# Performance work log

Hardware: AMD Instinct MI355X
Metric: run time of the kernel (lower is better)

## Reference

```python
import jax, jax.numpy as jnp
import numpy as np

B, C, L = 8, 512, 2048   # batch, input_dim (channels), sequence length
H = 8                    # multihead_cnt
K = 3                    # kernel_dim
DH = C // H              # per-head dim = 64
SCALE = 1.0 / float(np.sqrt(C))  # module divides by sqrt(input_dim), not sqrt(head_dim)


def _conv1d(x, w, b):
    # x: [B, C, L], w: [C_out, C_in, K], padding=1 keeps L
    y = jax.lax.conv_general_dilated(x, w, window_strides=(1,), padding=[(1, 1)],
                                     dimension_numbers=('NCH', 'OIH', 'NCH'))
    return y + b[None, :, None]


def setup_inputs() -> dict:
    key = jax.random.key(0)
    ks = jax.random.split(key, 7)
    x = jax.random.normal(ks[0], (B, C, L), dtype=jnp.float32)
    # xavier_normal_ std for Conv1d weight [C, C, K]: sqrt(2 / (fan_in + fan_out)), fan = C*K
    std = float(np.sqrt(2.0 / (C * K + C * K)))
    inp = {'x': x}
    for i in range(3):  # conv_cnt = 3 -> q, k, v convolutions
        inp[f'w{i}'] = jax.random.normal(ks[1 + 2 * i], (C, C, K), dtype=jnp.float32) * std
        inp[f'b{i}'] = jax.random.normal(ks[2 + 2 * i], (C,), dtype=jnp.float32) * 0.01
    return inp


def reference(x, w0, b0, w1, b1, w2, b2):
    # q, k, v projections via Conv1d (padding preserves length)
    q = _conv1d(x, w0, b0)  # [B, C, L]
    k = _conv1d(x, w1, b1)
    v = _conv1d(x, w2, b2)
    # torch.chunk along dim 1 == contiguous reshape into heads
    qh = q.reshape(B, H, DH, L)
    kh = k.reshape(B, H, DH, L)
    vh = v.reshape(B, H, DH, L)
    # scores = q^T k / sqrt(input_dim)  -> [B, H, L, L]
    scores = jnp.einsum('bhdl,bhdm->bhlm', qh, kh) * SCALE
    att = jax.nn.softmax(scores, axis=-1)
    # out = (att @ v^T)^T -> [B, H, DH, L]
    out = jnp.einsum('bhlm,bhdm->bhdl', att, vh)
    return out.reshape(B, C, L)
```

## Files before the change

### kernel.cpp

```cpp
#include <hip/hip_runtime.h>
#include <hip/hip_bf16.h>
#include <cstdint>

typedef unsigned short u16;
typedef short v8s __attribute__((ext_vector_type(8)));
typedef float v4f __attribute__((ext_vector_type(4)));
typedef u16 u16x8 __attribute__((ext_vector_type(8)));
typedef u16 u16x4 __attribute__((ext_vector_type(4)));

static constexpr int Bb = 8, Cc = 512, Ll = 2048, Hh = 8, Dh = 64;

__device__ __forceinline__ float bf2f(u16 u){
  unsigned x = ((unsigned)u) << 16; float f; __builtin_memcpy(&f, &x, 4); return f;
}
__device__ __forceinline__ u16 f2bf(float f){
  unsigned x; __builtin_memcpy(&x, &f, 4);
  x = (x + 0x7fffu + ((x >> 16) & 1u)) >> 16; return (u16)x;
}

__device__ __forceinline__ void async_cp16(const u16* g, u16* l){
  __builtin_amdgcn_global_load_lds(
      (const __attribute__((address_space(1))) unsigned int*)g,
      (__attribute__((address_space(3))) unsigned int*)l, 16, 0, 0);
}

#if __has_builtin(__builtin_amdgcn_exp2f)
#define EXP2F(x) __builtin_amdgcn_exp2f(x)
#else
#define EXP2F(x) exp2f(x)
#endif

__global__ __launch_bounds__(256) void detect_dtype(const u16* __restrict__ x, unsigned* __restrict__ flag){
  __shared__ int cnt;
  if (threadIdx.x == 0) cnt = 0;
  __syncthreads();
  int sane = 0;
  for (int i = threadIdx.x; i < 4096; i += 256){
    unsigned e = (x[2 * i] >> 7) & 0xFFu;
    sane += (e >= 90u && e <= 160u) ? 1 : 0;
  }
  atomicAdd(&cnt, sane);
  __syncthreads();
  if (threadIdx.x == 0) *flag = (cnt < 2458) ? 1u : 0u;
}

__global__ __launch_bounds__(256) void transpose_pad(const void* __restrict__ xv, const unsigned* __restrict__ flagp,
                                                     u16* __restrict__ xT){
  int b = blockIdx.z, ci0 = blockIdx.y * 64, l0 = blockIdx.x * 64;
  __shared__ u16 tb[64 * 72];
  const unsigned isf32 = *flagp;
  int t = threadIdx.x;
  int row = t >> 3, seg = t & 7;
  if (isf32){
    const float* xf = (const float*)xv;
    #pragma unroll
    for (int rnd = 0; rnd < 2; rnd++){
      int ci = row + rnd * 32;
      size_t off = ((size_t)(b * Cc + ci0 + ci)) * Ll + l0 + seg * 8;
      v4f a = *(const v4f*)(xf + off);
      v4f c4 = *(const v4f*)(xf + off + 4);
      #pragma unroll
      for (int j = 0; j < 4; j++) tb[(seg * 8 + j) * 72 + ci] = f2bf(a[j]);
      #pragma unroll
      for (int j = 0; j < 4; j++) tb[(seg * 8 + 4 + j) * 72 + ci] = f2bf(c4[j]);
    }
  } else {
    const u16* x = (const u16*)xv;
    #pragma unroll
    for (int rnd = 0; rnd < 2; rnd++){
      int ci = row + rnd * 32;
      u16x8 v = *(const u16x8*)(x + ((size_t)(b * Cc + ci0 + ci)) * Ll + l0 + seg * 8);
      #pragma unroll
      for (int j = 0; j < 8; j++) tb[(seg * 8 + j) * 72 + ci] = v[j];
    }
  }
  __syncthreads();
  #pragma unroll
  for (int rnd = 0; rnd < 2; rnd++){
    int l = row + rnd * 32;
    u16x8 v = *(const u16x8*)&tb[l * 72 + seg * 8];
    *(u16x8*)(xT + ((size_t)b * 2050 + 1 + l0 + l) * Cc + ci0 + seg * 8) = v;
  }
  if (blockIdx.x == 0 && t < 8){
    u16x8 z = {};
    *(u16x8*)(xT + ((size_t)b * 2050 + 0) * Cc + ci0 + t * 8) = z;
  }
  if (blockIdx.x == 31 && t < 8){
    u16x8 z = {};
    *(u16x8*)(xT + ((size_t)b * 2050 + 2049) * Cc + ci0 + t * 8) = z;
  }
}

__global__ __launch_bounds__(256) void pack_wb(const void* __restrict__ w0, const void* __restrict__ w1,
                                               const void* __restrict__ w2, const void* __restrict__ b0,
                                               const void* __restrict__ b1, const void* __restrict__ b2,
                                               const unsigned* __restrict__ flagp,
                                               u16* __restrict__ wp, u16* __restrict__ bb){
  int g = blockIdx.x * 256 + threadIdx.x;
  const unsigned isf32 = *flagp;
  if (g < 9 * 512 * 512){
    int ci = g & 511, co = (g >> 9) & 511, kc = g >> 18;
    int conv = kc / 3, k = kc - conv * 3;
    const void* w = (conv == 0) ? w0 : ((conv == 1) ? w1 : w2);
    size_t idx = (size_t)co * 1536 + ci * 3 + k;
    wp[g] = isf32 ? f2bf(((const float*)w)[idx]) : ((const u16*)w)[idx];
  } else {
    int g2 = g - 9 * 512 * 512;
    if (g2 < 1536){
      int conv = g2 >> 9, c = g2 & 511;
      const void* bsrc = (conv == 0) ? b0 : ((conv == 1) ? b1 : b2);
      bb[g2] = isf32 ? f2bf(((const float*)bsrc)[c]) : ((const u16*)bsrc)[c];
    }
  }
}

__global__ __launch_bounds__(256) void conv_gemm_fused(const u16* __restrict__ wp, const u16* __restrict__ xT,
                                                       const u16* __restrict__ bb, u16* __restrict__ qT,
                                                       u16* __restrict__ kT, u16* __restrict__ vN){
  int b = blockIdx.y, bx = blockIdx.x;
  int mt = bx >> 3, nt = bx & 7;
  int m0 = mt * 128, n0 = nt * 256;
  int conv = m0 >> 9;
  int co0 = m0 & 511;
  __shared__ u16 smem[12288 + 8256];
  u16* lA = smem;
  u16* lB = smem + 12288;
  int t = threadIdx.x, wave = t >> 6, lane = t & 63, quad = lane >> 4, lid = lane & 15;
  int wm = (wave >> 1) * 64, wn = (wave & 1) * 128;
  v4f acc[4][8] = {};
  const size_t xbase = (size_t)b * 2050 * Cc;

  for (int it = 0; it < 16; it++){
    int ci0 = it << 5;
    #pragma unroll
    for (int r = 0; r < 4; r++){
      int e = (r * 256 + t) * 8;
      int row = e >> 5, cio = e & 31;
      async_cp16(xT + xbase + (size_t)(n0 + row) * 512 + ci0 + cio, &lB[e]);
    }
    #pragma unroll
    for (int r = 0; r < 6; r++){
      int e = (r * 256 + t) * 8;
      int ks = e >> 12, rem = e & 4095, row = rem >> 5, cio = rem & 31;
      async_cp16(wp + ((size_t)((conv * 3 + ks) * 512 + co0 + row)) * 512 + ci0 + cio, &lA[e]);
    }
    if (t < 8){
      int hr = 256 + (t >> 2), cio = (t & 3) * 8;
      u16x8 hv = *(const u16x8*)(xT + xbase + (size_t)(n0 + hr) * 512 + ci0 + cio);
      *(u16x8*)&lB[hr * 32 + cio] = hv;
    }
    __syncthreads();
    #pragma unroll
    for (int ks = 0; ks < 3; ks++){
      v8s aF[4], bF[8];
      #pragma unroll
      for (int i = 0; i < 4; i++) aF[i] = *(const v8s*)&lA[ks * 4096 + (wm + i * 16 + lid) * 32 + quad * 8];
      #pragma unroll
      for (int j = 0; j < 8; j++) bF[j] = *(const v8s*)&lB[(wn + j * 16 + lid + ks) * 32 + quad * 8];
      #pragma unroll
      for (int i = 0; i < 4; i++)
        #pragma unroll
        for (int j = 0; j < 8; j++)
          acc[i][j] = __builtin_amdgcn_mfma_f32_16x16x32_bf16(aF[i], bF[j], acc[i][j], 0, 0, 0);
    }
    __syncthreads();
  }

  const float qsc = (float)(1.4426950408889634 / 22.627416997969522);
  if (conv < 2){
    u16* dst = (conv == 0) ? qT : kT;
    #pragma unroll
    for (int i = 0; i < 4; i++){
      int cog = m0 + wm + i * 16 + quad * 4;
      float bv[4];
      #pragma unroll
      for (int r = 0; r < 4; r++) bv[r] = bf2f(bb[cog + r]);
      int co = cog & 511;
      #pragma unroll
      for (int j = 0; j < 8; j++){
        int l = n0 + wn + j * 16 + lid;
        u16x4 pk;
        #pragma unroll
        for (int r = 0; r < 4; r++){
          float v = acc[i][j][r] + bv[r];
          if (conv == 0) v *= qsc;
          pk[r] = f2bf(v);
        }
        *(u16x4*)(dst + ((((size_t)b * Hh + (co >> 6)) * Ll + l) << 6) + (co & 63)) = pk;
      }
    }
  } else {
    u16* scr = smem;
    #pragma unroll
    for (int cs = 0; cs < 2; cs++){
      __syncthreads();
      #pragma unroll
      for (int i = 0; i < 4; i++){
        int cog = m0 + wm + i * 16 + quad * 4;
        float bv[4];
        #pragma unroll
        for (int r = 0; r < 4; r++) bv[r] = bf2f(bb[cog + r]);
        #pragma unroll
        for (int j = 0; j < 4; j++){
          int jj = cs * 4 + j;
          int lcl = (wave & 1) * 64 + j * 16 + lid;
          #pragma unroll
          for (int r = 0; r < 4; r++)
            scr[(wm + i * 16 + quad * 4 + r) * 130 + lcl] = f2bf(acc[i][jj][r] + bv[r]);
        }
      }
      __syncthreads();
      int row = t & 127, half = t >> 7;
      int co = co0 + row;
      size_t gb = (((size_t)b * Cc + co) << 11) + n0 + half * 128 + cs * 64;
      #pragma unroll
      for (int s = 0; s < 8; s++){
        u16x8 vv = *(const u16x8*)&scr[row * 130 + half * 64 + s * 8];
        *(u16x8*)(vN + gb + s * 8) = vv;
      }
    }
  }
}

__global__ __launch_bounds__(256) void attn_kernel(const u16* __restrict__ qT, const u16* __restrict__ kT,
                                                   const u16* __restrict__ vN, const unsigned* __restrict__ flagp,
                                                   void* __restrict__ outv){
  int bhx = blockIdx.x;
  int b = bhx >> 3, h = bhx & 7, l0 = blockIdx.y * 128;
  int t = threadIdx.x, w = t >> 6, lane = t & 63, quad = lane >> 4, lid = lane & 15;
  __shared__ u16 kls[128 * 72];
  __shared__ u16 vls[64 * 136];
  const unsigned isf32 = *flagp;
  const size_t bh = (size_t)b * Hh + h;

  int kadd[5], vadd[5];
  bool kval[5], vval[5];
  #pragma unroll
  for (int r = 0; r < 5; r++){
    int e = (r * 256 + t) * 8;
    kval[r] = e < 128 * 72;
    int slot = e / 72, off = e - slot * 72;
    int s5 = slot & 31;
    int m = (slot & ~31) | (((s5 >> 2) & 1) << 3) | (((s5 >> 3) & 1) << 4) | (((s5 >> 4) & 1) << 2) | (s5 & 3);
    kadd[r] = m * 64 + (off < 64 ? off : 0);
    vval[r] = e < 64 * 136;
    int d = e / 136, voff = e - d * 136;
    vadd[r] = d * Ll + (voff < 128 ? voff : 0);
  }
  const u16* kTb = kT + bh * Ll * 64;
  const u16* vNb = vN + ((size_t)(b * Cc + h * Dh)) * Ll;

  v8s qF[2][2];
  #pragma unroll
  for (int ci = 0; ci < 2; ci++)
    #pragma unroll
    for (int ks = 0; ks < 2; ks++)
      qF[ci][ks] = *(const v8s*)(qT + ((bh * Ll) + l0 + w * 32 + ci * 16 + lid) * 64 + ks * 32 + quad * 8);

  const v8s onesF = {0x3F80, 0x3F80, 0x3F80, 0x3F80, 0x3F80, 0x3F80, 0x3F80, 0x3F80};
  v4f o[2][4] = {};
  v4f o1[2] = {};

  for (int mt = 0; mt < 16; mt++){
    int m0 = mt * 128;
    const u16* kt = kTb + (size_t)m0 * 64;
    const u16* vt = vNb + m0;
    #pragma unroll
    for (int r = 0; r < 5; r++)
      if (kval[r]) async_cp16(kt + kadd[r], &kls[(r * 256 + t) * 8]);
    #pragma unroll
    for (int r = 0; r < 5; r++)
      if (vval[r]) async_cp16(vt + vadd[r], &vls[(r * 256 + t) * 8]);
    __syncthreads();

    v4f s[4][2][2] = {};
    #pragma unroll
    for (int ks = 0; ks < 2; ks++){
      v8s aF[4][2];
      #pragma unroll
      for (int c = 0; c < 4; c++)
        #pragma unroll
        for (int tt = 0; tt < 2; tt++)
          aF[c][tt] = *(const v8s*)&kls[(c * 32 + tt * 16 + lid) * 72 + ks * 32 + quad * 8];
      #pragma unroll
      for (int c = 0; c < 4; c++)
        #pragma unroll
        for (int tt = 0; tt < 2; tt++){
          s[c][tt][0] = __builtin_amdgcn_mfma_f32_16x16x32_bf16(aF[c][tt], qF[0][ks], s[c][tt][0], 0, 0, 0);
          s[c][tt][1] = __builtin_amdgcn_mfma_f32_16x16x32_bf16(aF[c][tt], qF[1][ks], s[c][tt][1], 0, 0, 0);
        }
    }

    #pragma unroll
    for (int c = 0; c < 4; c++){
      v8s aP[2];
      #pragma unroll
      for (int ci = 0; ci < 2; ci++){
        float p[8];
        #pragma unroll
        for (int tt = 0; tt < 2; tt++)
          #pragma unroll
          for (int r = 0; r < 4; r++)
            p[tt * 4 + r] = EXP2F(s[c][tt][ci][r]);
        unsigned u[4];
        #pragma unroll
        for (int k2 = 0; k2 < 4; k2++){
          __hip_bfloat162 hb = __float22bfloat162_rn(make_float2(p[2 * k2], p[2 * k2 + 1]));
          __builtin_memcpy(&u[k2], &hb, 4);
        }
        __builtin_memcpy(&aP[ci], u, 16);
      }
      v8s bV[4];
      #pragma unroll
      for (int df = 0; df < 4; df++)
        bV[df] = *(const v8s*)&vls[(df * 16 + lid) * 136 + c * 32 + quad * 8];
      #pragma unroll
      for (int ci = 0; ci < 2; ci++){
        #pragma unroll
        for (int df = 0; df < 4; df++)
          o[ci][df] = __builtin_amdgcn_mfma_f32_16x16x32_bf16(aP[ci], bV[df], o[ci][df], 0, 0, 0);
        o1[ci] = __builtin_amdgcn_mfma_f32_16x16x32_bf16(aP[ci], onesF, o1[ci], 0, 0, 0);
      }
    }
    __syncthreads();
  }

  #pragma unroll
  for (int lf = 0; lf < 2; lf++){
    v4f nv;
    #pragma unroll
    for (int r = 0; r < 4; r++) nv[r] = 1.f / o1[lf][r];
    #pragma unroll
    for (int df = 0; df < 4; df++){
      int d = df * 16 + lid;
      int l = l0 + w * 32 + lf * 16 + quad * 4;
      size_t ofs = (((bh << 6) + d) << 11) + l;
      if (isf32){
        v4f st;
        #pragma unroll
        for (int r = 0; r < 4; r++) st[r] = o[lf][df][r] * nv[r];
        *(v4f*)((float*)outv + ofs) = st;
      } else {
        u16x4 pk;
        #pragma unroll
        for (int r = 0; r < 4; r++) pk[r] = f2bf(o[lf][df][r] * nv[r]);
        *(u16x4*)((u16*)outv + ofs) = pk;
      }
    }
  }
}

extern "C" void kernel_launch(void* const* d_in, const int* in_sizes, int n_in,
                              void* d_out, int out_size, void* d_ws, size_t ws_size,
                              hipStream_t stream){
  const void* x  = d_in[0];
  const void* w0 = d_in[1];
  const void* b0 = d_in[2];
  const void* w1 = d_in[3];
  const void* b1 = d_in[4];
  const void* w2 = d_in[5];
  const void* b2 = d_in[6];
  u16* ws = (u16*)d_ws;
  unsigned* flag = (unsigned*)ws;
  u16* xT = ws + 64;
  u16* wp = xT + (size_t)8 * 2050 * 512;
  u16* bb = wp + (size_t)9 * 512 * 512;
  u16* qT = bb + 1536;
  u16* kT = qT + (size_t)8 * 8 * 2048 * 64;
  u16* vN = kT + (size_t)8 * 8 * 2048 * 64;

  detect_dtype<<<1, 256, 0, stream>>>((const u16*)x, flag);
  transpose_pad<<<dim3(32, 8, 8), 256, 0, stream>>>(x, flag, xT);
  pack_wb<<<dim3(9 * 512 * 512 / 256 + 6), 256, 0, stream>>>(w0, w1, w2, b0, b1, b2, flag, wp, bb);
  conv_gemm_fused<<<dim3(96, 8), 256, 0, stream>>>(wp, xT, bb, qT, kT, vN);
  attn_kernel<<<dim3(64, 16), 256, 0, stream>>>(qT, kT, vN, flag, d_out);
}
```

Before: 297.5 us.

## Double-buffer conv B tiles, read weights from global, prefetch attention K/V tiles

In the conv GEMM, the x tile is now double-buffered in LDS so the next tile's async copy overlaps the current MFMA work. The weight (A) operand is read straight from global memory instead of being staged through LDS, and the epilogue scratch stride changes from 130 to 136. In attention, V is double-buffered and the next K/V tiles are issued right after the QK^T phase, so the loads overlap the softmax and PV compute. The risks are added global-load latency on the weight fragments, and a possible race on K, since the next K tile is written into a single buffer while other waves may still be reading it.

```diff
diff --git a/kernel.cpp b/kernel.cpp
--- a/kernel.cpp
+++ b/kernel.cpp
@@ -122,41 +122,44 @@
   int m0 = mt * 128, n0 = nt * 256;
   int conv = m0 >> 9;
   int co0 = m0 & 511;
-  __shared__ u16 smem[12288 + 8256];
-  u16* lA = smem;
-  u16* lB = smem + 12288;
+  __shared__ u16 smem[17408];
   int t = threadIdx.x, wave = t >> 6, lane = t & 63, quad = lane >> 4, lid = lane & 15;
   int wm = (wave >> 1) * 64, wn = (wave & 1) * 128;
   v4f acc[4][8] = {};
   const size_t xbase = (size_t)b * 2050 * Cc;
-
-  for (int it = 0; it < 16; it++){
+  const u16* wbase = wp + ((size_t)(conv * 3) * 512 + co0) * 512;
+
+  auto stageB = [&](int it, u16* buf){
     int ci0 = it << 5;
     #pragma unroll
     for (int r = 0; r < 4; r++){
       int e = (r * 256 + t) * 8;
       int row = e >> 5, cio = e & 31;
-      async_cp16(xT + xbase + (size_t)(n0 + row) * 512 + ci0 + cio, &lB[e]);
-    }
-    #pragma unroll
-    for (int r = 0; r < 6; r++){
-      int e = (r * 256 + t) * 8;
-      int ks = e >> 12, rem = e & 4095, row = rem >> 5, cio = rem & 31;
-      async_cp16(wp + ((size_t)((conv * 3 + ks) * 512 + co0 + row)) * 512 + ci0 + cio, &lA[e]);
+      async_cp16(xT + xbase + (size_t)(n0 + row) * 512 + ci0 + cio, buf + e);
     }
     if (t < 8){
       int hr = 256 + (t >> 2), cio = (t & 3) * 8;
       u16x8 hv = *(const u16x8*)(xT + xbase + (size_t)(n0 + hr) * 512 + ci0 + cio);
-      *(u16x8*)&lB[hr * 32 + cio] = hv;
-    }
-    __syncthreads();
+      *(u16x8*)&buf[hr * 32 + cio] = hv;
+    }
+  };
+
+  stageB(0, smem);
+  __syncthreads();
+  for (int it = 0; it < 16; it++){
+    u16* cur = smem + (it & 1) * 8256;
+    if (it + 1 < 16) stageB(it + 1, smem + ((it + 1) & 1) * 8256);
+    int ci0 = it << 5;
     #pragma unroll
     for (int ks = 0; ks < 3; ks++){
       v8s aF[4], bF[8];
-      #pragma unroll
-      for (int i = 0; i < 4; i++) aF[i] = *(const v8s*)&lA[ks * 4096 + (wm + i * 16 + lid) * 32 + quad * 8];
-      #pragma unroll
-      for (int j = 0; j < 8; j++) bF[j] = *(const v8s*)&lB[(wn + j * 16 + lid + ks) * 32 + quad * 8];
+      const u16* wks = wbase + (size_t)ks * 512 * 512;
+      #pragma unroll
+      for (int i = 0; i < 4; i++)
+        aF[i] = *(const v8s*)(wks + (size_t)(wm + i * 16 + lid) * 512 + ci0 + quad * 8);
+      #pragma unroll
+      for (int j = 0; j < 8; j++)
+        bF[j] = *(const v8s*)&cur[(wn + j * 16 + lid + ks) * 32 + quad * 8];
       #pragma unroll
       for (int i = 0; i < 4; i++)
         #pragma unroll
@@ -206,7 +209,7 @@
           int lcl = (wave & 1) * 64 + j * 16 + lid;
           #pragma unroll
           for (int r = 0; r < 4; r++)
-            scr[(wm + i * 16 + quad * 4 + r) * 130 + lcl] = f2bf(acc[i][jj][r] + bv[r]);
+            scr[(wm + i * 16 + quad * 4 + r) * 136 + lcl] = f2bf(acc[i][jj][r] + bv[r]);
         }
       }
       __syncthreads();
@@ -215,7 +218,7 @@
       size_t gb = (((size_t)b * Cc + co) << 11) + n0 + half * 128 + cs * 64;
       #pragma unroll
       for (int s = 0; s < 8; s++){
-        u16x8 vv = *(const u16x8*)&scr[row * 130 + half * 64 + s * 8];
+        u16x8 vv = *(const u16x8*)&scr[row * 136 + half * 64 + s * 8];
         *(u16x8*)(vN + gb + s * 8) = vv;
       }
     }
@@ -229,7 +232,7 @@
   int b = bhx >> 3, h = bhx & 7, l0 = blockIdx.y * 128;
   int t = threadIdx.x, w = t >> 6, lane = t & 63, quad = lane >> 4, lid = lane & 15;
   __shared__ u16 kls[128 * 72];
-  __shared__ u16 vls[64 * 136];
+  __shared__ u16 vls[2 * 64 * 136];
   const unsigned isf32 = *flagp;
   const size_t bh = (size_t)b * Hh + h;
 
@@ -250,6 +253,13 @@
   const u16* kTb = kT + bh * Ll * 64;
   const u16* vNb = vN + ((size_t)(b * Cc + h * Dh)) * Ll;
 
+  #pragma unroll
+  for (int r = 0; r < 5; r++)
+    if (kval[r]) async_cp16(kTb + kadd[r], &kls[(r * 256 + t) * 8]);
+  #pragma unroll
+  for (int r = 0; r < 5; r++)
+    if (vval[r]) async_cp16(vNb + vadd[r], &vls[(r * 256 + t) * 8]);
+
   v8s qF[2][2];
   #pragma unroll
   for (int ci = 0; ci < 2; ci++)
@@ -260,19 +270,9 @@
   const v8s onesF = {0x3F80, 0x3F80, 0x3F80, 0x3F80, 0x3F80, 0x3F80, 0x3F80, 0x3F80};
   v4f o[2][4] = {};
   v4f o1[2] = {};
+  __syncthreads();
 
   for (int mt = 0; mt < 16; mt++){
-    int m0 = mt * 128;
-    const u16* kt = kTb + (size_t)m0 * 64;
-    const u16* vt = vNb + m0;
-    #pragma unroll
-    for (int r = 0; r < 5; r++)
-      if (kval[r]) async_cp16(kt + kadd[r], &kls[(r * 256 + t) * 8]);
-    #pragma unroll
-    for (int r = 0; r < 5; r++)
-      if (vval[r]) async_cp16(vt + vadd[r], &vls[(r * 256 + t) * 8]);
-    __syncthreads();
-
     v4f s[4][2][2] = {};
     #pragma unroll
     for (int ks = 0; ks < 2; ks++){
@@ -290,7 +290,21 @@
           s[c][tt][1] = __builtin_amdgcn_mfma_f32_16x16x32_bf16(aF[c][tt], qF[1][ks], s[c][tt][1], 0, 0, 0);
         }
     }
-
+    __syncthreads();
+
+    if (mt + 1 < 16){
+      const u16* kt = kTb + (size_t)(mt + 1) * 128 * 64;
+      const u16* vt = vNb + (mt + 1) * 128;
+      u16* vdst = vls + ((mt + 1) & 1) * (64 * 136);
+      #pragma unroll
+      for (int r = 0; r < 5; r++)
+        if (kval[r]) async_cp16(kt + kadd[r], &kls[(r * 256 + t) * 8]);
+      #pragma unroll
+      for (int r = 0; r < 5; r++)
+        if (vval[r]) async_cp16(vt + vadd[r], &vdst[(r * 256 + t) * 8]);
+    }
+
+    const u16* vcur = vls + (mt & 1) * (64 * 136);
     #pragma unroll
     for (int c = 0; c < 4; c++){
       v8s aP[2];
@@ -313,7 +327,7 @@
       v8s bV[4];
       #pragma unroll
       for (int df = 0; df < 4; df++)
-        bV[df] = *(const v8s*)&vls[(df * 16 + lid) * 136 + c * 32 + quad * 8];
+        bV[df] = *(const v8s*)&vcur[(df * 16 + lid) * 136 + c * 32 + quad * 8];
       #pragma unroll
       for (int ci = 0; ci < 2; ci++){
         #pragma unroll
```

Measured after the change: 311.8 us. 1.05x slower.
